# Optimization experiments

Hardware: AMD Instinct MI355X
Metric: run time of the kernel (lower is better)

Reference implementation:

```python
import jax, jax.numpy as jnp
import numpy as np

N = 100000   # nodes
E = 800000   # edges
D = 128      # input dim
H = 128      # hidden dim
C = 2        # output classes
BN_EPS = 1e-5


def setup_inputs() -> dict:
    key = jax.random.key(0)
    ks = jax.random.split(key, 24)
    glorot = lambda k, shape: jax.random.normal(k, shape, dtype=jnp.float32) * np.sqrt(2.0 / (shape[0] + shape[1]))
    inp = {
        "x": jax.random.normal(ks[0], (N, D), dtype=jnp.float32),
        "edge_index": jax.random.randint(ks[1], (2, E), 0, N, dtype=jnp.int64),
        "W0": glorot(ks[2], (D, H)), "b0": jnp.zeros((H,), jnp.float32),
        "W1": glorot(ks[3], (H, H)), "b1": jnp.zeros((H,), jnp.float32),
        "W2": glorot(ks[4], (H, H)), "b2": jnp.zeros((H,), jnp.float32),
        "W3": glorot(ks[5], (H, C)), "b3": jnp.zeros((C,), jnp.float32),
        # BatchNorm (eval mode: running stats)
        "bn0_g": jax.random.normal(ks[6], (H,), dtype=jnp.float32) * 0.1 + 1.0,
        "bn0_b": jax.random.normal(ks[7], (H,), dtype=jnp.float32) * 0.1,
        "bn0_m": jax.random.normal(ks[8], (H,), dtype=jnp.float32) * 0.1,
        "bn0_v": jax.random.uniform(ks[9], (H,), dtype=jnp.float32) + 0.5,
        "bn1_g": jax.random.normal(ks[10], (H,), dtype=jnp.float32) * 0.1 + 1.0,
        "bn1_b": jax.random.normal(ks[11], (H,), dtype=jnp.float32) * 0.1,
        "bn1_m": jax.random.normal(ks[12], (H,), dtype=jnp.float32) * 0.1,
        "bn1_v": jax.random.uniform(ks[13], (H,), dtype=jnp.float32) + 0.5,
    }
    return inp


def _gcn_conv(h, W, b, src, dst, norm, self_norm):
    # GCNConv: D^-1/2 (A + I) D^-1/2 (h W) + b
    hw = h @ W                                             # [N, out]
    msg = hw[src] * norm[:, None]                          # [E, out] gather
    agg = jax.ops.segment_sum(msg, dst, num_segments=N)    # [N, out] scatter-add
    return agg + hw * self_norm[:, None] + b


def _bn_eval(h, g, b, m, v):
    return (h - m) * (g * jax.lax.rsqrt(v + BN_EPS)) + b


def reference(x, edge_index, W0, b0, W1, b1, W2, b2, W3, b3,
              bn0_g, bn0_b, bn0_m, bn0_v, bn1_g, bn1_b, bn1_m, bn1_v):
    src, dst = edge_index[0], edge_index[1]
    # symmetric normalization with self-loops
    deg = jax.ops.segment_sum(jnp.ones((E,), jnp.float32), dst, num_segments=N) + 1.0
    dis = jax.lax.rsqrt(deg)                 # deg >= 1, no inf
    norm = dis[src] * dis[dst]               # per-edge norm
    self_norm = dis * dis                    # self-loop norm

    # layer 0 (eval mode: dropout is identity)
    h = jax.nn.relu(_gcn_conv(x, W0, b0, src, dst, norm, self_norm))
    # layer 1: conv -> bn -> relu -> residual
    h_prev = h
    h = _gcn_conv(h, W1, b1, src, dst, norm, self_norm)
    h = jax.nn.relu(_bn_eval(h, bn0_g, bn0_b, bn0_m, bn0_v)) + h_prev
    # layer 2
    h_prev = h
    h = _gcn_conv(h, W2, b2, src, dst, norm, self_norm)
    h = jax.nn.relu(_bn_eval(h, bn1_g, bn1_b, bn1_m, bn1_v)) + h_prev
    # output layer
    h = _gcn_conv(h, W3, b3, src, dst, norm, self_norm)
    return jax.nn.log_softmax(h, axis=1)
```

## Files before the change

### kernel.cpp

```cpp
#include <hip/hip_runtime.h>
#include <hip/hip_bf16.h>
#include <type_traits>

#define NN 100000
#define NE 800000
#define HD 128
#define BN_EPS 1e-5f

typedef __bf16 bf16x8 __attribute__((ext_vector_type(8)));
typedef float  f32x4  __attribute__((ext_vector_type(4)));
typedef float  f32x2  __attribute__((ext_vector_type(2)));


__global__ __launch_bounds__(256) void count_k(const int* __restrict__ ei, int* __restrict__ count,
                                               int* __restrict__ rank) {
    int e = blockIdx.x * 256 + threadIdx.x;
    if (e < NE) rank[e] = atomicAdd(&count[ei[NE + e]], 1);
}

__global__ __launch_bounds__(256) void bnpre_k(const float* __restrict__ g0, const float* __restrict__ b0,
                                               const float* __restrict__ m0, const float* __restrict__ v0,
                                               const float* __restrict__ g1, const float* __restrict__ b1,
                                               const float* __restrict__ m1, const float* __restrict__ v1,
                                               float* __restrict__ A0, float* __restrict__ B0,
                                               float* __restrict__ A1, float* __restrict__ B1) {
    int t = threadIdx.x;
    if (t < 128) {
        float a = g0[t] * rsqrtf(v0[t] + BN_EPS);
        A0[t] = a; B0[t] = b0[t] - m0[t] * a;
    } else {
        int u = t - 128;
        float a = g1[u] * rsqrtf(v1[u] + BN_EPS);
        A1[u] = a; B1[u] = b1[u] - m1[u] * a;
    }
}

__global__ __launch_bounds__(256) void prepw_k(const float* __restrict__ W0, const float* __restrict__ W1,
                                               const float* __restrict__ W2, __bf16* __restrict__ WT) {
    const float* Ws[3] = {W0, W1, W2};
    const float* W = Ws[blockIdx.x];
    __bf16* T = WT + blockIdx.x * (HD * HD);
    int tid = threadIdx.x;
    #pragma unroll
    for (int it = 0; it < 64; ++it) {
        int idx = it * 256 + tid;
        int n = idx >> 7, k = idx & 127;
        T[idx] = (__bf16)W[k * HD + n];
    }
}

__global__ __launch_bounds__(256) void scan1_k(const int* __restrict__ count,
                                               int* __restrict__ rp, int* __restrict__ bsums,
                                               float* __restrict__ dis, float* __restrict__ selfn) {
    __shared__ int sm[256];
    int tid = threadIdx.x;
    int i = blockIdx.x * 256 + tid;
    int v = (i < NN) ? count[i] : 0;
    if (i < NN) {
        float deg = (float)v + 1.0f;
        float di = rsqrtf(deg);
        dis[i] = di;
        selfn[i] = di * di;
    }
    sm[tid] = v; __syncthreads();
    for (int off = 1; off < 256; off <<= 1) {
        int t = (tid >= off) ? sm[tid - off] : 0;
        __syncthreads();
        sm[tid] += t;
        __syncthreads();
    }
    if (i < NN) rp[i] = sm[tid] - v;
    if (tid == 255) bsums[blockIdx.x] = sm[tid];
}

__global__ __launch_bounds__(512) void scan2_k(int* __restrict__ bsums, int nb) {
    __shared__ int sm[512];
    int tid = threadIdx.x;
    int v = (tid < nb) ? bsums[tid] : 0;
    sm[tid] = v; __syncthreads();
    for (int off = 1; off < 512; off <<= 1) {
        int t = (tid >= off) ? sm[tid - off] : 0;
        __syncthreads();
        sm[tid] += t;
        __syncthreads();
    }
    if (tid < nb) bsums[tid] = sm[tid] - v;
}

__global__ __launch_bounds__(256) void scan3_k(int* __restrict__ rp, const int* __restrict__ bsums) {
    int i = blockIdx.x * 256 + threadIdx.x;
    if (i < NN) rp[i] += bsums[blockIdx.x];
    if (i == 0) rp[NN] = NE;
}

__global__ __launch_bounds__(256) void scatter_k(const int* __restrict__ ei, const int* __restrict__ rp,
                                                 const int* __restrict__ rank, const float* __restrict__ dis,
                                                 uint2* __restrict__ edges) {
    int e = blockIdx.x * 256 + threadIdx.x;
    if (e >= NE) return;
    int s = ei[e], d = ei[NE + e];
    int pos = rp[d] + rank[e];
    edges[pos] = make_uint2((unsigned)s, __float_as_uint(dis[s] * dis[d]));
}


#define WROW 136

template <typename T>
__global__ __launch_bounds__(256, 4) void gemm128_k(const T* __restrict__ A, const __bf16* __restrict__ WTg,
                                                    __bf16* __restrict__ HW) {
    __shared__ __bf16 WL[128 * WROW];
    const int tid = threadIdx.x;
    const int wid  = __builtin_amdgcn_readfirstlane(tid >> 6);
    const int lane = tid & 63;
    const int m = lane & 15, quad = lane >> 4;
    const int row_base = blockIdx.x * 64 + wid * 16;

    int r = row_base + m;
    if (r >= NN) r = NN - 1;
    bf16x8 afr[4];
    if constexpr (std::is_same<T, float>::value) {
        const float4* ap = (const float4*)(A + (size_t)r * HD);
        #pragma unroll
        for (int ks = 0; ks < 4; ++ks) {
            float4 x0 = ap[ks * 8 + quad * 2], x1 = ap[ks * 8 + quad * 2 + 1];
            bf16x8 a;
            a[0] = (__bf16)x0.x; a[1] = (__bf16)x0.y; a[2] = (__bf16)x0.z; a[3] = (__bf16)x0.w;
            a[4] = (__bf16)x1.x; a[5] = (__bf16)x1.y; a[6] = (__bf16)x1.z; a[7] = (__bf16)x1.w;
            afr[ks] = a;
        }
    } else {
        const bf16x8* ap = (const bf16x8*)(A + (size_t)r * HD);
        #pragma unroll
        for (int ks = 0; ks < 4; ++ks) afr[ks] = ap[ks * 4 + quad];
    }

    #pragma unroll
    for (int it = 0; it < 8; ++it) {
        int id = it * 256 + tid;
        int n = id >> 4, c = id & 15;
        *(uint4*)&WL[n * WROW + c * 8] = *(const uint4*)(WTg + n * HD + c * 8);
    }
    __syncthreads();

    f32x4 acc[8];
    #pragma unroll
    for (int ct = 0; ct < 8; ++ct) acc[ct] = (f32x4){0.f, 0.f, 0.f, 0.f};

    #pragma unroll
    for (int ks = 0; ks < 4; ++ks) {
        const int k0 = ks * 32 + quad * 8;
        #pragma unroll
        for (int ct = 0; ct < 8; ++ct) {
            bf16x8 bfr = *(const bf16x8*)&WL[(ct * 16 + m) * WROW + k0];
            acc[ct] = __builtin_amdgcn_mfma_f32_16x16x32_bf16(afr[ks], bfr, acc[ct], 0, 0, 0);
        }
    }

    #pragma unroll
    for (int ct = 0; ct < 8; ++ct)
        #pragma unroll
        for (int rr = 0; rr < 4; ++rr) {
            int row = row_base + quad * 4 + rr;
            if (row < NN) HW[(size_t)row * HD + ct * 16 + m] = (__bf16)acc[ct][rr];
        }
}


__device__ __forceinline__ void acc8p(f32x2* acc, uint4 rv, float wt) {
    f32x2 w2 = {wt, wt};
    f32x2 x0 = {__uint_as_float(rv.x << 16), __uint_as_float(rv.x & 0xffff0000u)};
    f32x2 x1 = {__uint_as_float(rv.y << 16), __uint_as_float(rv.y & 0xffff0000u)};
    f32x2 x2 = {__uint_as_float(rv.z << 16), __uint_as_float(rv.z & 0xffff0000u)};
    f32x2 x3 = {__uint_as_float(rv.w << 16), __uint_as_float(rv.w & 0xffff0000u)};
    acc[0] = __builtin_elementwise_fma(x0, w2, acc[0]);
    acc[1] = __builtin_elementwise_fma(x1, w2, acc[1]);
    acc[2] = __builtin_elementwise_fma(x2, w2, acc[2]);
    acc[3] = __builtin_elementwise_fma(x3, w2, acc[3]);
}

__device__ __forceinline__ void unpack8(uint4 rv, float* f) {
    f[0] = __uint_as_float(rv.x << 16);         f[1] = __uint_as_float(rv.x & 0xffff0000u);
    f[2] = __uint_as_float(rv.y << 16);         f[3] = __uint_as_float(rv.y & 0xffff0000u);
    f[4] = __uint_as_float(rv.z << 16);         f[5] = __uint_as_float(rv.z & 0xffff0000u);
    f[6] = __uint_as_float(rv.w << 16);         f[7] = __uint_as_float(rv.w & 0xffff0000u);
}

template <int MODE>
__global__ __launch_bounds__(256) void agg_k(const __bf16* __restrict__ hw, const int* __restrict__ rp,
                                             const uint2* __restrict__ edges,
                                             const float* __restrict__ selfn, const float* __restrict__ bias,
                                             const float* __restrict__ bnA, const float* __restrict__ bnB,
                                             __bf16* __restrict__ hb, const float* __restrict__ W3,
                                             float2* __restrict__ hw3) {
    const int lane = threadIdx.x & 63;
    const int wid  = threadIdx.x >> 6;
    const int grp  = lane >> 4;
    const int m    = lane & 15;
    const int n = blockIdx.x * 16 + wid * 4 + grp;
    const int c0 = m * 8;
    const int L = NE - 1;

    const int e0 = rp[n], e1 = rp[n + 1];

    const float sn = selfn[n];
    uint4 rv_self = *(const uint4*)(hw + ((size_t)n << 7) + c0);
    __bf16* hbp = hb + ((size_t)n << 7) + c0;
    uint4 rv_prev;
    if (MODE != 0) rv_prev = *(const uint4*)hbp;

    f32x2 acc2[4];
    #pragma unroll
    for (int j = 0; j < 4; ++j) acc2[j] = (f32x2){0.f, 0.f};

    int e = e0;
    int cnt = e1 - e0;
    uint2 edA = edges[min(e,     L)];
    uint2 edB = edges[min(e + 1, L)];
    uint2 edC = edges[min(e + 2, L)];
    uint2 edD = edges[min(e + 3, L)];
    while (cnt >= 4) {
        uint4 r0 = *(const uint4*)(hw + ((size_t)edA.x << 7) + c0);
        uint4 r1 = *(const uint4*)(hw + ((size_t)edB.x << 7) + c0);
        uint4 r2 = *(const uint4*)(hw + ((size_t)edC.x << 7) + c0);
        uint4 r3 = *(const uint4*)(hw + ((size_t)edD.x << 7) + c0);
        uint2 nA = edges[min(e + 4, L)];
        uint2 nB = edges[min(e + 5, L)];
        uint2 nC = edges[min(e + 6, L)];
        uint2 nD = edges[min(e + 7, L)];
        acc8p(acc2, r0, __uint_as_float(edA.y));
        acc8p(acc2, r1, __uint_as_float(edB.y));
        acc8p(acc2, r2, __uint_as_float(edC.y));
        acc8p(acc2, r3, __uint_as_float(edD.y));
        edA = nA; edB = nB; edC = nC; edD = nD;
        e += 4; cnt -= 4;
    }
    if (cnt >= 2) {
        uint4 r0 = *(const uint4*)(hw + ((size_t)edA.x << 7) + c0);
        uint4 r1 = *(const uint4*)(hw + ((size_t)edB.x << 7) + c0);
        acc8p(acc2, r0, __uint_as_float(edA.y));
        acc8p(acc2, r1, __uint_as_float(edB.y));
        edA = edC;
        cnt -= 2;
    }
    if (cnt == 1) {
        uint4 rv = *(const uint4*)(hw + ((size_t)edA.x << 7) + c0);
        acc8p(acc2, rv, __uint_as_float(edA.y));
    }
    acc8p(acc2, rv_self, sn);

    float acc[8] = {acc2[0][0], acc2[0][1], acc2[1][0], acc2[1][1],
                    acc2[2][0], acc2[2][1], acc2[3][0], acc2[3][1]};

    float4 bs0 = *(const float4*)(bias + c0);
    float4 bs1 = *(const float4*)(bias + c0 + 4);
    float z[8] = {acc[0] + bs0.x, acc[1] + bs0.y, acc[2] + bs0.z, acc[3] + bs0.w,
                  acc[4] + bs1.x, acc[5] + bs1.y, acc[6] + bs1.z, acc[7] + bs1.w};

    if (MODE == 0) {
        bf16x8 v;
        #pragma unroll
        for (int j = 0; j < 8; ++j) v[j] = (__bf16)fmaxf(z[j], 0.f);
        *(bf16x8*)hbp = v;
    } else {
        float4 a0v = *(const float4*)(bnA + c0), a1v = *(const float4*)(bnA + c0 + 4);
        float4 b0v = *(const float4*)(bnB + c0), b1v = *(const float4*)(bnB + c0 + 4);
        float Af[8] = {a0v.x, a0v.y, a0v.z, a0v.w, a1v.x, a1v.y, a1v.z, a1v.w};
        float Bf[8] = {b0v.x, b0v.y, b0v.z, b0v.w, b1v.x, b1v.y, b1v.z, b1v.w};
        float pr[8];
        unpack8(rv_prev, pr);
        float hn[8];
        #pragma unroll
        for (int j = 0; j < 8; ++j)
            hn[j] = fmaxf(fmaf(z[j], Af[j], Bf[j]), 0.f) + pr[j];

        if (MODE == 1) {
            bf16x8 v;
            #pragma unroll
            for (int j = 0; j < 8; ++j) v[j] = (__bf16)hn[j];
            *(bf16x8*)hbp = v;
        } else {
            float4 w0 = *(const float4*)(W3 + c0 * 2);
            float4 w1 = *(const float4*)(W3 + c0 * 2 + 4);
            float4 w2 = *(const float4*)(W3 + c0 * 2 + 8);
            float4 w3v = *(const float4*)(W3 + c0 * 2 + 12);
            float p0 = hn[0] * w0.x + hn[1] * w0.z + hn[2] * w1.x + hn[3] * w1.z
                     + hn[4] * w2.x + hn[5] * w2.z + hn[6] * w3v.x + hn[7] * w3v.z;
            float p1 = hn[0] * w0.y + hn[1] * w0.w + hn[2] * w1.y + hn[3] * w1.w
                     + hn[4] * w2.y + hn[5] * w2.w + hn[6] * w3v.y + hn[7] * w3v.w;
            #pragma unroll
            for (int o = 1; o < 16; o <<= 1) {
                p0 += __shfl_xor(p0, o);
                p1 += __shfl_xor(p1, o);
            }
            if (m == 0) hw3[n] = make_float2(p0, p1);
        }
    }
}


__global__ __launch_bounds__(256) void final_k(const float2* __restrict__ hw3, const int* __restrict__ rp,
                                               const uint2* __restrict__ edges,
                                               const float* __restrict__ selfn, const float* __restrict__ b3,
                                               float* __restrict__ out) {
    int n = blockIdx.x * 256 + threadIdx.x;
    if (n >= NN) return;
    float a0 = 0.f, a1 = 0.f;
    int e1 = rp[n + 1];
    for (int e = rp[n]; e < e1; ++e) {
        uint2 ed = edges[e];
        float w = __uint_as_float(ed.y);
        float2 v = hw3[ed.x];
        a0 = fmaf(w, v.x, a0);
        a1 = fmaf(w, v.y, a1);
    }
    float sn = selfn[n];
    float2 hv = hw3[n];
    float z0 = a0 + sn * hv.x + b3[0];
    float z1 = a1 + sn * hv.y + b3[1];
    float mx = fmaxf(z0, z1);
    float l = mx + logf(expf(z0 - mx) + expf(z1 - mx));
    out[n * 2 + 0] = z0 - l;
    out[n * 2 + 1] = z1 - l;
}


extern "C" void kernel_launch(void* const* d_in, const int* in_sizes, int n_in,
                              void* d_out, int out_size, void* d_ws, size_t ws_size,
                              hipStream_t stream) {
    (void)in_sizes; (void)n_in; (void)out_size; (void)ws_size;

    const float* x   = (const float*)d_in[0];
    const int*   ei  = (const int*)d_in[1];
    const float* W0  = (const float*)d_in[2];
    const float* b0  = (const float*)d_in[3];
    const float* W1  = (const float*)d_in[4];
    const float* b1  = (const float*)d_in[5];
    const float* W2  = (const float*)d_in[6];
    const float* b2  = (const float*)d_in[7];
    const float* W3  = (const float*)d_in[8];
    const float* b3  = (const float*)d_in[9];
    const float* bn0g = (const float*)d_in[10];
    const float* bn0b = (const float*)d_in[11];
    const float* bn0m = (const float*)d_in[12];
    const float* bn0v = (const float*)d_in[13];
    const float* bn1g = (const float*)d_in[14];
    const float* bn1b = (const float*)d_in[15];
    const float* bn1m = (const float*)d_in[16];
    const float* bn1v = (const float*)d_in[17];
    float* out = (float*)d_out;

    char* p = (char*)d_ws;
    auto alloc = [&](size_t bytes) -> void* {
        void* r = (void*)p;
        p += (bytes + 255) & ~(size_t)255;
        return r;
    };
    __bf16*  hb    = (__bf16*)alloc((size_t)NN * HD * 2);
    __bf16*  hw    = (__bf16*)alloc((size_t)NN * HD * 2);
    float2*  hw3   = (float2*)alloc((size_t)NN * 8);
    float*   dis   = (float*)alloc((size_t)NN * 4);
    float*   selfn = (float*)alloc((size_t)NN * 4);
    int*     count = (int*)alloc((size_t)NN * 4);
    int*     rp    = (int*)alloc((size_t)(NN + 1) * 4);
    uint2*   edges = (uint2*)alloc((size_t)NE * 8);
    int*     rank  = (int*)alloc((size_t)NE * 4);
    int*     bsums = (int*)alloc((size_t)512 * 4);
    float*   bnA0  = (float*)alloc(128 * 4);
    float*   bnB0  = (float*)alloc(128 * 4);
    float*   bnA1  = (float*)alloc(128 * 4);
    float*   bnB1  = (float*)alloc(128 * 4);
    __bf16*  WT    = (__bf16*)alloc((size_t)3 * HD * HD * 2);

    const int NB_E = (NE + 255) / 256;
    const int NB_N = (NN + 255) / 256;
    const int NB_G = (NN + 63) / 64;
    const int NB_A = (NN + 15) / 16;

    hipMemsetAsync(count, 0, (size_t)NN * 4, stream);

    count_k<<<NB_E, 256, 0, stream>>>(ei, count, rank);
    prepw_k<<<3, 256, 0, stream>>>(W0, W1, W2, WT);
    bnpre_k<<<1, 256, 0, stream>>>(bn0g, bn0b, bn0m, bn0v, bn1g, bn1b, bn1m, bn1v,
                                   bnA0, bnB0, bnA1, bnB1);
    scan1_k<<<NB_N, 256, 0, stream>>>(count, rp, bsums, dis, selfn);
    scan2_k<<<1, 512, 0, stream>>>(bsums, NB_N);
    scan3_k<<<NB_N, 256, 0, stream>>>(rp, bsums);
    scatter_k<<<NB_E, 256, 0, stream>>>(ei, rp, rank, dis, edges);

    gemm128_k<float><<<NB_G, 256, 0, stream>>>(x, WT, hw);
    agg_k<0><<<NB_A, 256, 0, stream>>>(hw, rp, edges, selfn, b0,
                                       nullptr, nullptr, hb, nullptr, nullptr);
    gemm128_k<__bf16><<<NB_G, 256, 0, stream>>>(hb, WT + HD * HD, hw);
    agg_k<1><<<NB_A, 256, 0, stream>>>(hw, rp, edges, selfn, b1,
                                       bnA0, bnB0, hb, nullptr, nullptr);
    gemm128_k<__bf16><<<NB_G, 256, 0, stream>>>(hb, WT + 2 * HD * HD, hw);
    agg_k<2><<<NB_A, 256, 0, stream>>>(hw, rp, edges, selfn, b2,
                                       bnA1, bnB1, hb, W3, hw3);
    final_k<<<NB_N, 256, 0, stream>>>(hw3, rp, edges, selfn, b3, out);
}
```

Baseline: 345.9 us.

## Merge prep and scan launches, software-pipeline edge loads in final kernel

Combines the weight-transpose and BatchNorm-precompute kernels into one launch. Fuses the second and third scan passes so each block reduces the preceding block sums itself, which drops a single-block serial kernel at the cost of redundant reads of the block sums. Unrolls the final aggregation loop by two and prefetches the next edge records, so more gathers are in flight per thread.

```diff
diff --git a/kernel.cpp b/kernel.cpp
--- a/kernel.cpp
+++ b/kernel.cpp
@@ -18,34 +18,34 @@
     if (e < NE) rank[e] = atomicAdd(&count[ei[NE + e]], 1);
 }
 
-__global__ __launch_bounds__(256) void bnpre_k(const float* __restrict__ g0, const float* __restrict__ b0,
-                                               const float* __restrict__ m0, const float* __restrict__ v0,
-                                               const float* __restrict__ g1, const float* __restrict__ b1,
-                                               const float* __restrict__ m1, const float* __restrict__ v1,
-                                               float* __restrict__ A0, float* __restrict__ B0,
-                                               float* __restrict__ A1, float* __restrict__ B1) {
-    int t = threadIdx.x;
-    if (t < 128) {
-        float a = g0[t] * rsqrtf(v0[t] + BN_EPS);
-        A0[t] = a; B0[t] = b0[t] - m0[t] * a;
+__global__ __launch_bounds__(256) void prep_k(const float* __restrict__ W0, const float* __restrict__ W1,
+                                              const float* __restrict__ W2, __bf16* __restrict__ WT,
+                                              const float* __restrict__ g0, const float* __restrict__ b0,
+                                              const float* __restrict__ m0, const float* __restrict__ v0,
+                                              const float* __restrict__ g1, const float* __restrict__ b1,
+                                              const float* __restrict__ m1, const float* __restrict__ v1,
+                                              float* __restrict__ A0, float* __restrict__ B0,
+                                              float* __restrict__ A1, float* __restrict__ B1) {
+    int tid = threadIdx.x;
+    if (blockIdx.x < 3) {
+        const float* Ws[3] = {W0, W1, W2};
+        const float* W = Ws[blockIdx.x];
+        __bf16* T = WT + blockIdx.x * (HD * HD);
+        #pragma unroll
+        for (int it = 0; it < 64; ++it) {
+            int idx = it * 256 + tid;
+            int n = idx >> 7, k = idx & 127;
+            T[idx] = (__bf16)W[k * HD + n];
+        }
     } else {
-        int u = t - 128;
-        float a = g1[u] * rsqrtf(v1[u] + BN_EPS);
-        A1[u] = a; B1[u] = b1[u] - m1[u] * a;
-    }
-}
-
-__global__ __launch_bounds__(256) void prepw_k(const float* __restrict__ W0, const float* __restrict__ W1,
-                                               const float* __restrict__ W2, __bf16* __restrict__ WT) {
-    const float* Ws[3] = {W0, W1, W2};
-    const float* W = Ws[blockIdx.x];
-    __bf16* T = WT + blockIdx.x * (HD * HD);
-    int tid = threadIdx.x;
-    #pragma unroll
-    for (int it = 0; it < 64; ++it) {
-        int idx = it * 256 + tid;
-        int n = idx >> 7, k = idx & 127;
-        T[idx] = (__bf16)W[k * HD + n];
+        if (tid < 128) {
+            float a = g0[tid] * rsqrtf(v0[tid] + BN_EPS);
+            A0[tid] = a; B0[tid] = b0[tid] - m0[tid] * a;
+        } else {
+            int u = tid - 128;
+            float a = g1[u] * rsqrtf(v1[u] + BN_EPS);
+            A1[u] = a; B1[u] = b1[u] - m1[u] * a;
+        }
     }
 }
 
@@ -73,23 +73,21 @@
     if (tid == 255) bsums[blockIdx.x] = sm[tid];
 }
 
-__global__ __launch_bounds__(512) void scan2_k(int* __restrict__ bsums, int nb) {
-    __shared__ int sm[512];
+__global__ __launch_bounds__(256) void scan23_k(int* __restrict__ rp, const int* __restrict__ bsums, int nb) {
+    __shared__ int sm[256];
     int tid = threadIdx.x;
-    int v = (tid < nb) ? bsums[tid] : 0;
-    sm[tid] = v; __syncthreads();
-    for (int off = 1; off < 512; off <<= 1) {
-        int t = (tid >= off) ? sm[tid - off] : 0;
+    int b = blockIdx.x;
+    int partial = 0;
+    for (int i = tid; i < b; i += 256) partial += bsums[i];
+    sm[tid] = partial; __syncthreads();
+    #pragma unroll
+    for (int off = 128; off > 0; off >>= 1) {
+        if (tid < off) sm[tid] += sm[tid + off];
         __syncthreads();
-        sm[tid] += t;
-        __syncthreads();
-    }
-    if (tid < nb) bsums[tid] = sm[tid] - v;
-}
-
-__global__ __launch_bounds__(256) void scan3_k(int* __restrict__ rp, const int* __restrict__ bsums) {
-    int i = blockIdx.x * 256 + threadIdx.x;
-    if (i < NN) rp[i] += bsums[blockIdx.x];
+    }
+    int prefix = sm[0];
+    int i = b * 256 + tid;
+    if (i < NN) rp[i] += prefix;
     if (i == 0) rp[NN] = NE;
 }
 
@@ -305,14 +303,27 @@
                                                float* __restrict__ out) {
     int n = blockIdx.x * 256 + threadIdx.x;
     if (n >= NN) return;
+    const int L = NE - 1;
     float a0 = 0.f, a1 = 0.f;
-    int e1 = rp[n + 1];
-    for (int e = rp[n]; e < e1; ++e) {
-        uint2 ed = edges[e];
-        float w = __uint_as_float(ed.y);
-        float2 v = hw3[ed.x];
-        a0 = fmaf(w, v.x, a0);
-        a1 = fmaf(w, v.y, a1);
+    int e0 = rp[n], e1 = rp[n + 1];
+    int cnt = e1 - e0;
+    uint2 edA = edges[min(e0,     L)];
+    uint2 edB = edges[min(e0 + 1, L)];
+    int e = e0;
+    while (cnt >= 2) {
+        float2 v0 = hw3[edA.x];
+        float2 v1 = hw3[edB.x];
+        float w0 = __uint_as_float(edA.y), w1 = __uint_as_float(edB.y);
+        edA = edges[min(e + 2, L)];
+        edB = edges[min(e + 3, L)];
+        a0 = fmaf(w0, v0.x, a0); a1 = fmaf(w0, v0.y, a1);
+        a0 = fmaf(w1, v1.x, a0); a1 = fmaf(w1, v1.y, a1);
+        e += 2; cnt -= 2;
+    }
+    if (cnt == 1) {
+        float2 v = hw3[edA.x];
+        float w = __uint_as_float(edA.y);
+        a0 = fmaf(w, v.x, a0); a1 = fmaf(w, v.y, a1);
     }
     float sn = selfn[n];
     float2 hv = hw3[n];
@@ -380,12 +391,11 @@
     hipMemsetAsync(count, 0, (size_t)NN * 4, stream);
 
     count_k<<<NB_E, 256, 0, stream>>>(ei, count, rank);
-    prepw_k<<<3, 256, 0, stream>>>(W0, W1, W2, WT);
-    bnpre_k<<<1, 256, 0, stream>>>(bn0g, bn0b, bn0m, bn0v, bn1g, bn1b, bn1m, bn1v,
-                                   bnA0, bnB0, bnA1, bnB1);
+    prep_k<<<4, 256, 0, stream>>>(W0, W1, W2, WT,
+                                  bn0g, bn0b, bn0m, bn0v, bn1g, bn1b, bn1m, bn1v,
+                                  bnA0, bnB0, bnA1, bnB1);
     scan1_k<<<NB_N, 256, 0, stream>>>(count, rp, bsums, dis, selfn);
-    scan2_k<<<1, 512, 0, stream>>>(bsums, NB_N);
-    scan3_k<<<NB_N, 256, 0, stream>>>(rp, bsums);
+    scan23_k<<<NB_N, 256, 0, stream>>>(rp, bsums, NB_N);
     scatter_k<<<NB_E, 256, 0, stream>>>(ei, rp, rank, dis, edges);
 
     gemm128_k<float><<<NB_G, 256, 0, stream>>>(x, WT, hw);
```

Result: no change. 340.2 us, median of 2 (-1.6%).
